# Optimization experiments

Hardware: AMD Instinct MI355X
Metric: run time of the kernel (lower is better)

Reference implementation:

```python
import jax, jax.numpy as jnp
import numpy as np

BETA = 0.9      # leak factor of snn.Leaky
THR = 1.0       # default threshold

# snntorch surrogate.atan(): forward = Heaviside(U), backward = (alpha/2)/(1+(pi/2*alpha*U)^2) with alpha=2 -> 1/(1+(pi*U)^2)
@jax.custom_vjp
def atan_spike(u):
    return (u > 0).astype(u.dtype)

def _atan_fwd(u):
    return atan_spike(u), u

def _atan_bwd(u, g):
    return (g / (1.0 + (jnp.pi * u) ** 2),)

atan_spike.defvjp(_atan_fwd, _atan_bwd)


def setup_inputs() -> dict:
    key = jax.random.key(0)
    k0, k1, k2 = jax.random.split(key, 3)
    T, B, H, W = 50, 128, 128, 128
    ni, nh, no = H * W, 256, 11
    x = jax.random.normal(k0, (T, B, H, W), dtype=jnp.float32)
    W1 = jax.random.normal(k1, (nh, ni), dtype=jnp.float32) / np.sqrt(ni).astype(np.float32)
    b1 = jnp.zeros((nh,), jnp.float32)
    W2 = jax.random.normal(k2, (no, nh), dtype=jnp.float32) / np.sqrt(nh).astype(np.float32)
    b2 = jnpphantom = None
    b2 = jnp.zeros((no,), jnp.float32)
    return {"x": x, "W1": W1, "b1": b1, "W2": W2, "b2": b2}


def reference(x, W1, b1, W2, b2):
    T, B = x.shape[0], x.shape[1]
    xf = x.reshape(T, B, -1)  # [T, B, 16384]

    def step(carry, xt):
        mem1, mem2 = carry
        cur1 = xt @ W1.T + b1                       # [B, nh]
        mem1 = BETA * mem1 + cur1
        spk1 = atan_spike(mem1 - THR)
        mem1 = mem1 - jax.lax.stop_gradient(spk1) * THR  # subtract reset (detached, as in snntorch)
        cur2 = spk1 @ W2.T + b2                     # [B, no]
        mem2 = BETA * mem2 + cur2
        spk2 = atan_spike(mem2 - THR)
        mem2 = mem2 - jax.lax.stop_gradient(spk2) * THR
        return (mem1, mem2), spk2

    mem1_0 = jnp.zeros((B, W1.shape[0]), x.dtype)
    mem2_0 = jnp.zeros((B, W2.shape[0]), x.dtype)
    _, spk2_rec = jax.lax.scan(step, (mem1_0, mem2_0), xf)
    return spk2_rec  # [T, B, 11]
```

## Files before the change

kernel.cpp:

```cpp
#include <hip/hip_runtime.h>


#define T_STEPS 50
#define BATCH   128
#define NI      16384
#define NH      256
#define NO      11
#define M_TOT   (T_STEPS * BATCH)
#define KSPLIT  8
#define KCHUNK  (NI / KSPLIT)
#define BK      32
#define KTILES  (KCHUNK / BK)
#define BM      128
#define BN      256

typedef _Float16 f16x8 __attribute__((ext_vector_type(8)));
typedef float    f32x4 __attribute__((ext_vector_type(4)));

__device__ __forceinline__ void split2(float f, _Float16& hi, _Float16& lo) {
    hi = (_Float16)f;
    lo = (_Float16)(f - (float)hi);
}

__global__ __launch_bounds__(256, 2) void gemm1_mfma(
    const float* __restrict__ X, const float* __restrict__ W1,
    float* __restrict__ part)
{
    __shared__ alignas(16) _Float16 Ah[BM * BK];
    __shared__ alignas(16) _Float16 Al[BM * BK];
    __shared__ alignas(16) _Float16 Bh[BN * BK];
    __shared__ alignas(16) _Float16 Bl[BN * BK];

    const int tid  = threadIdx.x;
    const int lane = tid & 63;
    const int wave = tid >> 6;
    const int wm   = wave >> 1;
    const int wn   = wave & 1;
    const int q    = lane >> 4;
    const int l15  = lane & 15;

    const int m0 = blockIdx.x * BM;
    const int ks = blockIdx.y;
    const int kbase = ks * KCHUNK;

    const int a_row[2] = { (tid + 0) >> 2, (tid + 256) >> 2 };
    const int a_g8 [2] = { (tid + 0) & 3,  (tid + 256) & 3 };
    int b_row[4], b_g8[4];
#pragma unroll
    for (int i = 0; i < 4; ++i) { b_row[i] = (tid + 256 * i) >> 2; b_g8[i] = (tid + 256 * i) & 3; }

    f32x4 acc[4][8];
#pragma unroll
    for (int im = 0; im < 4; ++im)
#pragma unroll
        for (int jn = 0; jn < 8; ++jn) acc[im][jn] = (f32x4){0.f, 0.f, 0.f, 0.f};

    for (int kt = 0; kt < KTILES; ++kt) {
        const int k0 = kbase + kt * BK;

        float av[2][8], bv[4][8];
#pragma unroll
        for (int i = 0; i < 2; ++i) {
            const float* s = X + (size_t)(m0 + a_row[i]) * NI + k0 + a_g8[i] * 8;
            float4 v0 = *(const float4*)s, v1 = *(const float4*)(s + 4);
            av[i][0]=v0.x; av[i][1]=v0.y; av[i][2]=v0.z; av[i][3]=v0.w;
            av[i][4]=v1.x; av[i][5]=v1.y; av[i][6]=v1.z; av[i][7]=v1.w;
        }
#pragma unroll
        for (int i = 0; i < 4; ++i) {
            const float* s = W1 + (size_t)b_row[i] * NI + k0 + b_g8[i] * 8;
            float4 v0 = *(const float4*)s, v1 = *(const float4*)(s + 4);
            bv[i][0]=v0.x; bv[i][1]=v0.y; bv[i][2]=v0.z; bv[i][3]=v0.w;
            bv[i][4]=v1.x; bv[i][5]=v1.y; bv[i][6]=v1.z; bv[i][7]=v1.w;
        }

        f16x8 ahv[2], alv[2], bhv[4], blv[4];
#pragma unroll
        for (int i = 0; i < 2; ++i)
#pragma unroll
            for (int j = 0; j < 8; ++j) { _Float16 h, l; split2(av[i][j], h, l); ahv[i][j] = h; alv[i][j] = l; }
#pragma unroll
        for (int i = 0; i < 4; ++i)
#pragma unroll
            for (int j = 0; j < 8; ++j) { _Float16 h, l; split2(bv[i][j], h, l); bhv[i][j] = h; blv[i][j] = l; }

        __syncthreads();

#pragma unroll
        for (int i = 0; i < 2; ++i) {
            const int off = a_row[i] * BK + a_g8[i] * 8;
            *(f16x8*)&Ah[off] = ahv[i];
            *(f16x8*)&Al[off] = alv[i];
        }
#pragma unroll
        for (int i = 0; i < 4; ++i) {
            const int off = b_row[i] * BK + b_g8[i] * 8;
            *(f16x8*)&Bh[off] = bhv[i];
            *(f16x8*)&Bl[off] = blv[i];
        }

        __syncthreads();

        f16x8 fah[4], fal[4], fbh[8], fbl[8];
#pragma unroll
        for (int im = 0; im < 4; ++im) {
            const int off = (64 * wm + 16 * im + l15) * BK + q * 8;
            fah[im] = *(const f16x8*)&Ah[off];
            fal[im] = *(const f16x8*)&Al[off];
        }
#pragma unroll
        for (int jn = 0; jn < 8; ++jn) {
            const int off = (128 * wn + 16 * jn + l15) * BK + q * 8;
            fbh[jn] = *(const f16x8*)&Bh[off];
            fbl[jn] = *(const f16x8*)&Bl[off];
        }
#pragma unroll
        for (int im = 0; im < 4; ++im)
#pragma unroll
            for (int jn = 0; jn < 8; ++jn) {
                acc[im][jn] = __builtin_amdgcn_mfma_f32_16x16x32_f16(fah[im], fbh[jn], acc[im][jn], 0, 0, 0);
                acc[im][jn] = __builtin_amdgcn_mfma_f32_16x16x32_f16(fal[im], fbh[jn], acc[im][jn], 0, 0, 0);
                acc[im][jn] = __builtin_amdgcn_mfma_f32_16x16x32_f16(fah[im], fbl[jn], acc[im][jn], 0, 0, 0);
            }
    }

    float* P = part + (size_t)ks * M_TOT * NH;
#pragma unroll
    for (int im = 0; im < 4; ++im) {
        const int mrow = m0 + 64 * wm + 16 * im + 4 * q;
#pragma unroll
        for (int jn = 0; jn < 8; ++jn) {
            const int n = 128 * wn + 16 * jn + l15;
#pragma unroll
            for (int r = 0; r < 4; ++r)
                P[(size_t)(mrow + r) * NH + n] = acc[im][jn][r];
        }
    }
}

__global__ __launch_bounds__(256) void scan1_kernel(
    const float* __restrict__ part, const float* __restrict__ b1,
    float* __restrict__ spk1)
{
    const int b = blockIdx.x;
    const int h = threadIdx.x;
    const float bias = b1[h];
    const size_t S = (size_t)M_TOT * NH;
    float mem = 0.f;
    for (int t = 0; t < T_STEPS; ++t) {
        const size_t idx = ((size_t)(t * BATCH + b)) * NH + h;
        float c = ((part[idx] + part[S + idx]) + (part[2 * S + idx] + part[3 * S + idx]))
                + ((part[4 * S + idx] + part[5 * S + idx]) + (part[6 * S + idx] + part[7 * S + idx]));
        c += bias;
        mem = __fadd_rn(__fmul_rn(0.9f, mem), c);
        const float s = (mem > 1.0f) ? 1.0f : 0.0f;
        mem -= s;
        spk1[idx] = s;
    }
}

__global__ __launch_bounds__(256) void gemm2_kernel(
    const float* __restrict__ spk1, const float* __restrict__ W2,
    const float* __restrict__ b2, float* __restrict__ cur2)
{
    const int wave = threadIdx.x >> 6;
    const int lane = threadIdx.x & 63;
    const int m = blockIdx.x * 4 + wave;
    const float4 s4 = *(const float4*)(spk1 + (size_t)m * NH + (lane << 2));
#pragma unroll
    for (int o = 0; o < NO; ++o) {
        const float4 w4 = *(const float4*)(W2 + (size_t)o * NH + (lane << 2));
        float p = (s4.x * w4.x + s4.y * w4.y) + (s4.z * w4.z + s4.w * w4.w);
#pragma unroll
        for (int d = 32; d; d >>= 1) p += __shfl_xor(p, d, 64);
        if (lane == 0) cur2[(size_t)m * 16 + o] = p + b2[o];
    }
}

__global__ __launch_bounds__(256) void scan2_kernel(
    const float* __restrict__ cur2, float* __restrict__ out)
{
    const int tid = blockIdx.x * 256 + threadIdx.x;
    if (tid >= BATCH * NO) return;
    const int b = tid / NO, o = tid % NO;
    float mem = 0.f;
    for (int t = 0; t < T_STEPS; ++t) {
        const float c = cur2[(size_t)(t * BATCH + b) * 16 + o];
        mem = __fadd_rn(__fmul_rn(0.9f, mem), c);
        const float s = (mem > 1.0f) ? 1.0f : 0.0f;
        mem -= s;
        out[(size_t)(t * BATCH + b) * NO + o] = s;
    }
}

extern "C" void kernel_launch(void* const* d_in, const int* in_sizes, int n_in,
                              void* d_out, int out_size, void* d_ws, size_t ws_size,
                              hipStream_t stream) {
    const float* x  = (const float*)d_in[0];
    const float* W1 = (const float*)d_in[1];
    const float* b1 = (const float*)d_in[2];
    const float* W2 = (const float*)d_in[3];
    const float* b2 = (const float*)d_in[4];
    float* out = (float*)d_out;

    float* part = (float*)d_ws;
    float* spk1 = part + (size_t)KSPLIT * M_TOT * NH;
    float* cur2 = spk1 + (size_t)M_TOT * NH;

    dim3 g1(M_TOT / BM, KSPLIT);
    gemm1_mfma<<<g1, 256, 0, stream>>>(x, W1, part);
    scan1_kernel<<<BATCH, NH, 0, stream>>>(part, b1, spk1);
    gemm2_kernel<<<M_TOT / 4, 256, 0, stream>>>(spk1, W2, b2, cur2);
    scan2_kernel<<<(BATCH * NO + 255) / 256, 256, 0, stream>>>(cur2, out);
}
```

Before: 682.8 us.

## Pre-split W1 to fp16 hi/lo, stream it direct to LDS, swizzle LDS

```diff
diff --git a/kernel.cpp b/kernel.cpp
--- a/kernel.cpp
+++ b/kernel.cpp
@@ -15,6 +15,7 @@
 #define BN      256
 
 typedef _Float16 f16x8 __attribute__((ext_vector_type(8)));
+typedef _Float16 f16x4 __attribute__((ext_vector_type(4)));
 typedef float    f32x4 __attribute__((ext_vector_type(4)));
 
 __device__ __forceinline__ void split2(float f, _Float16& hi, _Float16& lo) {
@@ -22,9 +23,36 @@
     lo = (_Float16)(f - (float)hi);
 }
 
+__device__ __forceinline__ int swz(int row, int blk) {
+    return row * BK + ((blk ^ ((row >> 1) & 3)) << 3);
+}
+
+typedef __attribute__((address_space(1))) const unsigned int guint;
+typedef __attribute__((address_space(3))) unsigned int luint;
+__device__ __forceinline__ void lds16(const void* g, void* l) {
+    __builtin_amdgcn_global_load_lds((guint*)g, (luint*)l, 16, 0, 0);
+}
+
+__global__ __launch_bounds__(256) void convert_w1(
+    const float* __restrict__ W1, _Float16* __restrict__ Wh, _Float16* __restrict__ Wl)
+{
+    const size_t i = ((size_t)blockIdx.x * 256 + threadIdx.x) * 4;
+    const float4 v = *(const float4*)(W1 + i);
+    float a[4] = { v.x, v.y, v.z, v.w };
+    f16x4 h, l;
+#pragma unroll
+    for (int j = 0; j < 4; ++j) {
+        _Float16 hh, ll;
+        split2(a[j], hh, ll);
+        h[j] = hh; l[j] = ll;
+    }
+    *(f16x4*)(Wh + i) = h;
+    *(f16x4*)(Wl + i) = l;
+}
+
 __global__ __launch_bounds__(256, 2) void gemm1_mfma(
-    const float* __restrict__ X, const float* __restrict__ W1,
-    float* __restrict__ part)
+    const float* __restrict__ X, const _Float16* __restrict__ W1h,
+    const _Float16* __restrict__ W1l, float* __restrict__ part)
 {
     __shared__ alignas(16) _Float16 Ah[BM * BK];
     __shared__ alignas(16) _Float16 Al[BM * BK];
@@ -43,85 +71,76 @@
     const int ks = blockIdx.y;
     const int kbase = ks * KCHUNK;
 
-    const int a_row[2] = { (tid + 0) >> 2, (tid + 256) >> 2 };
-    const int a_g8 [2] = { (tid + 0) & 3,  (tid + 256) & 3 };
-    int b_row[4], b_g8[4];
-#pragma unroll
-    for (int i = 0; i < 4; ++i) { b_row[i] = (tid + 256 * i) >> 2; b_g8[i] = (tid + 256 * i) & 3; }
+    const int a_row[2] = { tid >> 2, 64 + (tid >> 2) };
+    const int a_g8     = tid & 3;
+
+    int b_row[4], b_fb[4];
+#pragma unroll
+    for (int j = 0; j < 4; ++j) {
+        b_row[j] = wave * 64 + j * 16 + (lane >> 2);
+        b_fb[j]  = (lane & 3) ^ ((b_row[j] >> 1) & 3);
+    }
 
     f32x4 acc[4][8];
 #pragma unroll
     for (int im = 0; im < 4; ++im)
 #pragma unroll
         for (int jn = 0; jn < 8; ++jn) acc[im][jn] = (f32x4){0.f, 0.f, 0.f, 0.f};
+
+    const int xsw = (l15 >> 1) & 3;
+    const int qx  = (q ^ xsw) << 3;
 
     for (int kt = 0; kt < KTILES; ++kt) {
         const int k0 = kbase + kt * BK;
 
-        float av[2][8], bv[4][8];
+        f16x8 ahv[2], alv[2];
 #pragma unroll
         for (int i = 0; i < 2; ++i) {
-            const float* s = X + (size_t)(m0 + a_row[i]) * NI + k0 + a_g8[i] * 8;
-            float4 v0 = *(const float4*)s, v1 = *(const float4*)(s + 4);
-            av[i][0]=v0.x; av[i][1]=v0.y; av[i][2]=v0.z; av[i][3]=v0.w;
-            av[i][4]=v1.x; av[i][5]=v1.y; av[i][6]=v1.z; av[i][7]=v1.w;
-        }
-#pragma unroll
-        for (int i = 0; i < 4; ++i) {
-            const float* s = W1 + (size_t)b_row[i] * NI + k0 + b_g8[i] * 8;
-            float4 v0 = *(const float4*)s, v1 = *(const float4*)(s + 4);
-            bv[i][0]=v0.x; bv[i][1]=v0.y; bv[i][2]=v0.z; bv[i][3]=v0.w;
-            bv[i][4]=v1.x; bv[i][5]=v1.y; bv[i][6]=v1.z; bv[i][7]=v1.w;
-        }
-
-        f16x8 ahv[2], alv[2], bhv[4], blv[4];
-#pragma unroll
-        for (int i = 0; i < 2; ++i)
-#pragma unroll
-            for (int j = 0; j < 8; ++j) { _Float16 h, l; split2(av[i][j], h, l); ahv[i][j] = h; alv[i][j] = l; }
-#pragma unroll
-        for (int i = 0; i < 4; ++i)
-#pragma unroll
-            for (int j = 0; j < 8; ++j) { _Float16 h, l; split2(bv[i][j], h, l); bhv[i][j] = h; blv[i][j] = l; }
+            const float* s = X + (size_t)(m0 + a_row[i]) * NI + k0 + a_g8 * 8;
+            const float4 v0 = *(const float4*)s, v1 = *(const float4*)(s + 4);
+            float av[8] = { v0.x, v0.y, v0.z, v0.w, v1.x, v1.y, v1.z, v1.w };
+#pragma unroll
+            for (int j = 0; j < 8; ++j) { _Float16 h, l; split2(av[j], h, l); ahv[i][j] = h; alv[i][j] = l; }
+        }
 
         __syncthreads();
 
 #pragma unroll
+        for (int j = 0; j < 4; ++j) {
+            const size_t goff = (size_t)b_row[j] * NI + k0 + b_fb[j] * 8;
+            const int lbase = (wave * 4 + j) * 512;
+            lds16(W1h + goff, &Bh[lbase]);
+            lds16(W1l + goff, &Bl[lbase]);
+        }
+
+#pragma unroll
         for (int i = 0; i < 2; ++i) {
-            const int off = a_row[i] * BK + a_g8[i] * 8;
+            const int off = swz(a_row[i], a_g8);
             *(f16x8*)&Ah[off] = ahv[i];
             *(f16x8*)&Al[off] = alv[i];
         }
-#pragma unroll
-        for (int i = 0; i < 4; ++i) {
-            const int off = b_row[i] * BK + b_g8[i] * 8;
-            *(f16x8*)&Bh[off] = bhv[i];
-            *(f16x8*)&Bl[off] = blv[i];
-        }
 
         __syncthreads();
 
-        f16x8 fah[4], fal[4], fbh[8], fbl[8];
+        f16x8 fah[4], fal[4];
 #pragma unroll
         for (int im = 0; im < 4; ++im) {
-            const int off = (64 * wm + 16 * im + l15) * BK + q * 8;
+            const int off = (64 * wm + 16 * im + l15) * BK + qx;
             fah[im] = *(const f16x8*)&Ah[off];
             fal[im] = *(const f16x8*)&Al[off];
         }
 #pragma unroll
         for (int jn = 0; jn < 8; ++jn) {
-            const int off = (128 * wn + 16 * jn + l15) * BK + q * 8;
-            fbh[jn] = *(const f16x8*)&Bh[off];
-            fbl[jn] = *(const f16x8*)&Bl[off];
-        }
-#pragma unroll
-        for (int im = 0; im < 4; ++im)
-#pragma unroll
-            for (int jn = 0; jn < 8; ++jn) {
-                acc[im][jn] = __builtin_amdgcn_mfma_f32_16x16x32_f16(fah[im], fbh[jn], acc[im][jn], 0, 0, 0);
-                acc[im][jn] = __builtin_amdgcn_mfma_f32_16x16x32_f16(fal[im], fbh[jn], acc[im][jn], 0, 0, 0);
-                acc[im][jn] = __builtin_amdgcn_mfma_f32_16x16x32_f16(fah[im], fbl[jn], acc[im][jn], 0, 0, 0);
+            const int off = (128 * wn + 16 * jn + l15) * BK + qx;
+            const f16x8 fbh = *(const f16x8*)&Bh[off];
+            const f16x8 fbl = *(const f16x8*)&Bl[off];
+#pragma unroll
+            for (int im = 0; im < 4; ++im) {
+                acc[im][jn] = __builtin_amdgcn_mfma_f32_16x16x32_f16(fah[im], fbh, acc[im][jn], 0, 0, 0);
+                acc[im][jn] = __builtin_amdgcn_mfma_f32_16x16x32_f16(fal[im], fbh, acc[im][jn], 0, 0, 0);
+                acc[im][jn] = __builtin_amdgcn_mfma_f32_16x16x32_f16(fah[im], fbl, acc[im][jn], 0, 0, 0);
             }
+        }
     }
 
     float* P = part + (size_t)ks * M_TOT * NH;
@@ -206,9 +225,12 @@
     float* part = (float*)d_ws;
     float* spk1 = part + (size_t)KSPLIT * M_TOT * NH;
     float* cur2 = spk1 + (size_t)M_TOT * NH;
-
+    _Float16* W1h = (_Float16*)(cur2 + (size_t)M_TOT * 16);
+    _Float16* W1l = W1h + (size_t)NH * NI;
+
+    convert_w1<<<(NH * NI) / (256 * 4), 256, 0, stream>>>(W1, W1h, W1l);
     dim3 g1(M_TOT / BM, KSPLIT);
-    gemm1_mfma<<<g1, 256, 0, stream>>>(x, W1, part);
+    gemm1_mfma<<<g1, 256, 0, stream>>>(x, W1h, W1l, part);
     scan1_kernel<<<BATCH, NH, 0, stream>>>(part, b1, spk1);
     gemm2_kernel<<<M_TOT / 4, 256, 0, stream>>>(spk1, W2, b2, cur2);
     scan2_kernel<<<(BATCH * NO + 255) / 256, 256, 0, stream>>>(cur2, out);
```

New measurement: 674.7 us. No clear change (-1.2%).
